# Kernel tuning notes

Measured on AMD Instinct MI355X. Metric: run time of the kernel, lower is better.

The kernel has to match this reference:

```python
import jax, jax.numpy as jnp
import numpy as np

D_MODEL = 768
N_HEADS = 4
N_POINTS = 4
PATCH = 16
IMG = 224
HF = IMG // PATCH  # 14
WF = IMG // PATCH  # 14
LQ = HF * WF       # 196 tokens
DH = D_MODEL // N_HEADS  # 192


def setup_inputs() -> dict:
    key = jax.random.key(0)
    ks = jax.random.split(key, 14)
    s = 0.02
    inp = {
        "x": jax.random.normal(ks[0], (4, 16, 3, IMG, IMG), dtype=jnp.float32),
        # patch-embed conv (Conv2d 3->768, k=16, s=16)
        "embed_w": s * jax.random.normal(ks[1], (D_MODEL, 3, PATCH, PATCH), dtype=jnp.float32),
        "embed_b": jnp.zeros((D_MODEL,), dtype=jnp.float32),
        # MSDeformAttn linears (nn.Linear stores W as [out, in]; y = x @ W.T + b)
        "value_w": s * jax.random.normal(ks[2], (D_MODEL, D_MODEL), dtype=jnp.float32),
        "value_b": jnp.zeros((D_MODEL,), dtype=jnp.float32),
        "off_w": s * jax.random.normal(ks[3], (N_HEADS * N_POINTS * 2, D_MODEL), dtype=jnp.float32),
        "off_b": s * jax.random.normal(ks[4], (N_HEADS * N_POINTS * 2,), dtype=jnp.float32),
        "aw_w": s * jax.random.normal(ks[5], (N_HEADS * N_POINTS, D_MODEL), dtype=jnp.float32),
        "aw_b": jnp.zeros((N_HEADS * N_POINTS,), dtype=jnp.float32),
        "outp_w": s * jax.random.normal(ks[6], (D_MODEL, D_MODEL), dtype=jnp.float32),
        "outp_b": jnp.zeros((D_MODEL,), dtype=jnp.float32),
        # final nn.Linear proj
        "proj_w": s * jax.random.normal(ks[7], (D_MODEL, D_MODEL), dtype=jnp.float32),
        "proj_b": jnp.zeros((D_MODEL,), dtype=jnp.float32),
    }
    return inp


def _patch_embed(x, w, b):
    # x: (N,3,H,W); non-overlapping 16x16 patches == Conv2d(3,D,16,16)
    N = x.shape[0]
    xh = x.reshape(N, 3, HF, PATCH, WF, PATCH)
    feat = jnp.einsum('nchpwq,dcpq->nhwd', xh, w) + b  # (N,HF,WF,D)
    return feat.reshape(N, LQ, D_MODEL)


def _ref_points():
    lin = jnp.linspace(0.0, 1.0, HF)
    gy, gx = jnp.meshgrid(lin, lin, indexing='ij')
    return jnp.stack([gx, gy], -1).reshape(LQ, 2)  # (Lq, 2) in [0,1], (x,y)


def _deform_attn_core(value, loc, attn):
    # value: (N, Lq, M, Dh); loc: (N, Lq, M, P, 2) normalized [0,1]; attn: (N, Lq, M, P)
    N = value.shape[0]
    # grid_sample align_corners=False: pixel = (2*loc-1 + 1)*S/2 - 0.5 = loc*S - 0.5
    px = loc[..., 0] * WF - 0.5
    py = loc[..., 1] * HF - 0.5
    x0 = jnp.floor(px).astype(jnp.int32)
    y0 = jnp.floor(py).astype(jnp.int32)
    x1, y1 = x0 + 1, y0 + 1
    wx1 = px - x0.astype(px.dtype)
    wy1 = py - y0.astype(py.dtype)
    wx0, wy0 = 1.0 - wx1, 1.0 - wy1

    valh = value.transpose(0, 2, 1, 3)  # (N, M, HW, Dh)

    def gather(ix, iy):
        valid = (ix >= 0) & (ix < WF) & (iy >= 0) & (iy < HF)  # zeros padding
        idx = jnp.clip(iy, 0, HF - 1) * WF + jnp.clip(ix, 0, WF - 1)
        idxm = idx.transpose(0, 2, 1, 3).reshape(N, N_HEADS, LQ * N_POINTS)
        g = jnp.take_along_axis(valh, idxm[..., None], axis=2)  # (N,M,Lq*P,Dh)
        g = g * valid.transpose(0, 2, 1, 3).reshape(N, N_HEADS, LQ * N_POINTS, 1)
        return g.reshape(N, N_HEADS, LQ, N_POINTS, DH)

    def w4(a, b):  # (N,Lq,M,P) -> (N,M,Lq,P,1)
        return (a * b).transpose(0, 2, 1, 3)[..., None]

    sampled = (w4(wx0, wy0) * gather(x0, y0) + w4(wx1, wy0) * gather(x1, y0)
               + w4(wx0, wy1) * gather(x0, y1) + w4(wx1, wy1) * gather(x1, y1))
    # weighted combine over points
    out = (sampled * attn.transpose(0, 2, 1, 3)[..., None]).sum(3)  # (N,M,Lq,Dh)
    return out.transpose(0, 2, 1, 3).reshape(N, LQ, D_MODEL)


def reference(x, embed_w, embed_b, value_w, value_b, off_w, off_b, aw_w, aw_b,
              outp_w, outp_b, proj_w, proj_b):
    B, T = x.shape[0], x.shape[1]
    N = B * T
    xi = x.reshape(N, 3, IMG, IMG)
    feat = _patch_embed(xi, embed_w, embed_b)  # (N, Lq, D)

    # MSDeformAttn (n_levels=1)
    value = (feat @ value_w.T + value_b).reshape(N, LQ, N_HEADS, DH)
    off = (feat @ off_w.T + off_b).reshape(N, LQ, N_HEADS, N_POINTS, 2)
    aw = (feat @ aw_w.T + aw_b).reshape(N, LQ, N_HEADS, N_POINTS)
    aw = jax.nn.softmax(aw, axis=-1)  # softmax over n_levels*n_points = 4

    ref = _ref_points()  # (Lq, 2)
    norm = jnp.array([WF, HF], dtype=feat.dtype)  # offset_normalizer = (W, H)
    loc = ref[None, :, None, None, :] + off / norm  # (N,Lq,M,P,2)

    out = _deform_attn_core(value, loc, aw)
    out = out @ outp_w.T + outp_b  # output_proj

    pooled = out.mean(axis=1)  # mean over tokens
    final = pooled @ proj_w.T + proj_b
    return final.reshape(B, T, D_MODEL)
```

## Files before the change

### kernel.cpp

```cpp
#include <hip/hip_runtime.h>
#include <hip/hip_bf16.h>


using bf16 = __bf16;
typedef bf16  bf16x8 __attribute__((ext_vector_type(8)));
typedef float f32x4  __attribute__((ext_vector_type(4)));

#define N_IMG   64
#define LQ      196
#define DM      768
#define NH      4
#define DH      192
#define M_ROWS  (N_IMG * LQ)
#define NCAT    896

#define OFF_A     ((size_t)0)
#define OFF_FEAT  (OFF_A    + 19267584)
#define OFF_WEMB  (OFF_FEAT + 19267584)
#define OFF_WCAT  (OFF_WEMB + 1179648)
#define OFF_BCAT  (OFF_WCAT + 1376256)
#define OFF_VBUF  (OFF_BCAT + 4096)
#define OFF_OA    (OFF_VBUF + 19267584)
#define OFF_CORE  (OFF_OA   + 3211264)
#define OFF_POOL  (OFF_CORE + 196608)

__device__ __forceinline__ void gload_lds16(const bf16* g, bf16* l) {
#if __has_builtin(__builtin_amdgcn_global_load_lds)
  __builtin_amdgcn_global_load_lds(
      (const __attribute__((address_space(1))) void*)g,
      (__attribute__((address_space(3))) void*)l, 16, 0, 0);
#else
  *(bf16x8*)l = *(const bf16x8*)g;
#endif
}

__global__ void stage_kernel(const float* __restrict__ x,
                             const float* __restrict__ embed_w,
                             const float* __restrict__ value_w,
                             const float* __restrict__ off_w,
                             const float* __restrict__ aw_w,
                             const float* __restrict__ value_b,
                             const float* __restrict__ off_b,
                             const float* __restrict__ aw_b,
                             bf16* __restrict__ A,
                             bf16* __restrict__ Wemb, bf16* __restrict__ Wcat,
                             float* __restrict__ bcat, float* __restrict__ core) {
  const int bid = blockIdx.x;
  if (bid < 9408) {
    const int t   = bid * 256 + threadIdx.x;
    const int row = t / 192;
    const int j   = t - row * 192;
    const int k   = j * 4;
    const int c   = k >> 8;
    const int r   = k & 255;
    const int p   = r >> 4;
    const int q   = r & 15;
    const int n   = row / 196;
    const int lq  = row - n * 196;
    const int h   = lq / 14;
    const int w   = lq - h * 14;
    const float4 v = *(const float4*)(x +
        ((((size_t)n * 3 + c) * 224) + h * 16 + p) * 224 + w * 16 + q);
    bf16* dst = A + (size_t)row * DM + k;
    dst[0] = (bf16)v.x; dst[1] = (bf16)v.y; dst[2] = (bf16)v.z; dst[3] = (bf16)v.w;
    return;
  }
  const int idx = (bid - 9408) * 256 + threadIdx.x;
  if (idx < DM * DM) Wemb[idx] = (bf16)embed_w[idx];
  {
    int rr = idx / DM, kk = idx - rr * DM;
    float v = 0.f;
    if (rr < 768)       v = value_w[idx];
    else if (rr < 800)  v = off_w[(rr - 768) * DM + kk];
    else if (rr < 816)  v = aw_w[(rr - 800) * DM + kk];
    Wcat[idx] = (bf16)v;
  }
  if (idx < NCAT) {
    float v = 0.f;
    if (idx < 768)      v = value_b[idx];
    else if (idx < 800) v = off_b[idx - 768];
    else if (idx < 816) v = aw_b[idx - 800];
    bcat[idx] = v;
  }
  if (idx < N_IMG * DM) core[idx] = 0.f;
}

template <typename OutT>
__global__ void gemm_bt(const bf16* __restrict__ A, const bf16* __restrict__ B,
                        const float* __restrict__ bias, OutT* __restrict__ C,
                        int M, int N, int K) {
  __shared__ bf16 As[128 * 64];
  __shared__ bf16 Bs[128 * 64];

  const int tid  = threadIdx.x;
  const int wave = tid >> 6;
  const int lane = tid & 63;
  const int nBase = blockIdx.x * 128;
  const int mBase = blockIdx.y * 128;
  const int wm = wave & 1;
  const int wn = wave >> 1;
  const int quad = lane >> 4;
  const int r16  = lane & 15;

  const f32x4 zero = {0.f, 0.f, 0.f, 0.f};
  f32x4 acc[4][4];
#pragma unroll
  for (int mi = 0; mi < 4; ++mi)
#pragma unroll
    for (int ni = 0; ni < 4; ++ni) acc[mi][ni] = zero;

  const int srow = wave * 32 + (lane >> 3);
  const int scol = (lane & 7) * 8;
  const bf16* Ag = A + (size_t)(mBase + srow) * K + scol;
  const bf16* Bg = B + (size_t)(nBase + srow) * K + scol;
  bf16* Al = As + srow * 64 + scol;
  bf16* Bl = Bs + srow * 64 + scol;

  for (int kt = 0; kt < K; kt += 64) {
#pragma unroll
    for (int i = 0; i < 4; ++i) {
      gload_lds16(Ag + (size_t)(i * 8) * K + kt, Al + i * 8 * 64);
      gload_lds16(Bg + (size_t)(i * 8) * K + kt, Bl + i * 8 * 64);
    }
    __syncthreads();
#pragma unroll
    for (int kk = 0; kk < 64; kk += 32) {
      bf16x8 af[4], bfr[4];
#pragma unroll
      for (int mi = 0; mi < 4; ++mi)
        af[mi] = *(const bf16x8*)&As[(wm * 64 + mi * 16 + r16) * 64 + kk + quad * 8];
#pragma unroll
      for (int ni = 0; ni < 4; ++ni)
        bfr[ni] = *(const bf16x8*)&Bs[(wn * 64 + ni * 16 + r16) * 64 + kk + quad * 8];
#pragma unroll
      for (int mi = 0; mi < 4; ++mi)
#pragma unroll
        for (int ni = 0; ni < 4; ++ni)
          acc[mi][ni] = __builtin_amdgcn_mfma_f32_16x16x32_bf16(
              af[mi], bfr[ni], acc[mi][ni], 0, 0, 0);
    }
    __syncthreads();
  }

#pragma unroll
  for (int ni = 0; ni < 4; ++ni) {
    const int col = nBase + wn * 64 + ni * 16 + r16;
    const float bv = bias[col];
#pragma unroll
    for (int mi = 0; mi < 4; ++mi) {
      const int row0 = mBase + wm * 64 + mi * 16 + quad * 4;
#pragma unroll
      for (int rr = 0; rr < 4; ++rr) {
        float v = acc[mi][ni][rr] + bv;
        C[(size_t)(row0 + rr) * N + col] = (OutT)v;
      }
    }
  }
}

__global__ void gemm2_mixed(const bf16* __restrict__ A, const bf16* __restrict__ B,
                            const float* __restrict__ bias,
                            bf16* __restrict__ Vb, float* __restrict__ OA,
                            int M, int N, int K) {
  __shared__ bf16 As[128 * 64];
  __shared__ bf16 Bs[128 * 64];

  const int tid  = threadIdx.x;
  const int wave = tid >> 6;
  const int lane = tid & 63;
  const int nBase = blockIdx.x * 128;
  const int mBase = blockIdx.y * 128;
  const int wm = wave & 1;
  const int wn = wave >> 1;
  const int quad = lane >> 4;
  const int r16  = lane & 15;

  const f32x4 zero = {0.f, 0.f, 0.f, 0.f};
  f32x4 acc[4][4];
#pragma unroll
  for (int mi = 0; mi < 4; ++mi)
#pragma unroll
    for (int ni = 0; ni < 4; ++ni) acc[mi][ni] = zero;

  const int srow = wave * 32 + (lane >> 3);
  const int scol = (lane & 7) * 8;
  const bf16* Ag = A + (size_t)(mBase + srow) * K + scol;
  const bf16* Bg = B + (size_t)(nBase + srow) * K + scol;
  bf16* Al = As + srow * 64 + scol;
  bf16* Bl = Bs + srow * 64 + scol;

  for (int kt = 0; kt < K; kt += 64) {
#pragma unroll
    for (int i = 0; i < 4; ++i) {
      gload_lds16(Ag + (size_t)(i * 8) * K + kt, Al + i * 8 * 64);
      gload_lds16(Bg + (size_t)(i * 8) * K + kt, Bl + i * 8 * 64);
    }
    __syncthreads();
#pragma unroll
    for (int kk = 0; kk < 64; kk += 32) {
      bf16x8 af[4], bfr[4];
#pragma unroll
      for (int mi = 0; mi < 4; ++mi)
        af[mi] = *(const bf16x8*)&As[(wm * 64 + mi * 16 + r16) * 64 + kk + quad * 8];
#pragma unroll
      for (int ni = 0; ni < 4; ++ni)
        bfr[ni] = *(const bf16x8*)&Bs[(wn * 64 + ni * 16 + r16) * 64 + kk + quad * 8];
#pragma unroll
      for (int mi = 0; mi < 4; ++mi)
#pragma unroll
        for (int ni = 0; ni < 4; ++ni)
          acc[mi][ni] = __builtin_amdgcn_mfma_f32_16x16x32_bf16(
              af[mi], bfr[ni], acc[mi][ni], 0, 0, 0);
    }
    __syncthreads();
  }

#pragma unroll
  for (int ni = 0; ni < 4; ++ni) {
    const int col = nBase + wn * 64 + ni * 16 + r16;
    const float bv = bias[col];
#pragma unroll
    for (int mi = 0; mi < 4; ++mi) {
      const int row0 = mBase + wm * 64 + mi * 16 + quad * 4;
#pragma unroll
      for (int rr = 0; rr < 4; ++rr) {
        float v = acc[mi][ni][rr] + bv;
        int row = row0 + rr;
        if (col < 768) {
          Vb[(size_t)row * 768 + col] = (bf16)v;
        } else if (col < 816) {
          OA[(size_t)row * 64 + (col - 768)] = v;
        }
      }
    }
  }
}

__global__ void deform_kernel(const bf16* __restrict__ Vb,
                              const float* __restrict__ OA,
                              float* __restrict__ core) {
  __shared__ float s_w[64][4];
  __shared__ int   s_t[64][4];

  const int n   = blockIdx.x;
  const int lq0 = blockIdx.y * 4;
  const int z   = blockIdx.z;
  const int tid = threadIdx.x;

  if (tid < 64) {
    const int i = tid >> 4;
    const int m = (tid >> 2) & 3;
    const int p = tid & 3;
    const int lq = lq0 + i;
    const float* row = OA + ((size_t)n * LQ + lq) * 64;

    const float l0 = row[32 + m * 4 + 0];
    const float l1 = row[32 + m * 4 + 1];
    const float l2 = row[32 + m * 4 + 2];
    const float l3 = row[32 + m * 4 + 3];
    const float mx = fmaxf(fmaxf(l0, l1), fmaxf(l2, l3));
    const float e0 = __expf(l0 - mx), e1 = __expf(l1 - mx);
    const float e2 = __expf(l2 - mx), e3 = __expf(l3 - mx);
    const float inv = 1.f / (e0 + e1 + e2 + e3);
    const float ep[4] = {e0, e1, e2, e3};
    const float ew = ep[p] * inv;

    const int h = lq / 14, w = lq - (lq / 14) * 14;
    const float px = (float)w * (14.f / 13.f) - 0.5f + row[(m * 4 + p) * 2 + 0];
    const float py = (float)h * (14.f / 13.f) - 0.5f + row[(m * 4 + p) * 2 + 1];
    const float fx = floorf(px), fy = floorf(py);
    const int x0 = (int)fx, y0 = (int)fy;
    const float wx1 = px - fx, wy1 = py - fy;
    const float wx0 = 1.f - wx1, wy0 = 1.f - wy1;

    const bool vx0 = (x0 >= 0) & (x0 < 14);
    const bool vx1 = (x0 >= -1) & (x0 < 13);
    const bool vy0 = (y0 >= 0) & (y0 < 14);
    const bool vy1 = (y0 >= -1) & (y0 < 13);
    const int cx0 = min(max(x0, 0), 13),      cx1 = min(max(x0 + 1, 0), 13);
    const int cy0 = min(max(y0, 0), 13) * 14, cy1 = min(max(y0 + 1, 0), 13) * 14;

    s_w[tid][0] = (vx0 & vy0) ? ew * wx0 * wy0 : 0.f;
    s_w[tid][1] = (vx1 & vy0) ? ew * wx1 * wy0 : 0.f;
    s_w[tid][2] = (vx0 & vy1) ? ew * wx0 * wy1 : 0.f;
    s_w[tid][3] = (vx1 & vy1) ? ew * wx1 * wy1 : 0.f;
    s_t[tid][0] = cy0 + cx0;
    s_t[tid][1] = cy0 + cx1;
    s_t[tid][2] = cy1 + cx0;
    s_t[tid][3] = cy1 + cx1;
  }
  __syncthreads();

  const int ch = z * 256 + tid;
  const int m  = ch / DH;
  const bf16* vb = Vb + (size_t)n * LQ * 768 + ch;
  float acc = 0.f;
#pragma unroll
  for (int i = 0; i < 4; ++i) {
#pragma unroll
    for (int p = 0; p < 4; ++p) {
      const int e = i * 16 + m * 4 + p;
      const float4 w4 = *(const float4*)s_w[e];
      const int4   t4 = *(const int4*)s_t[e];
      acc += w4.x * (float)vb[(size_t)t4.x * 768];
      acc += w4.y * (float)vb[(size_t)t4.y * 768];
      acc += w4.z * (float)vb[(size_t)t4.z * 768];
      acc += w4.w * (float)vb[(size_t)t4.w * 768];
    }
  }
  atomicAdd(&core[(size_t)n * DM + ch], acc * (1.f / 196.f));
}

__global__ void small_linear(const float* __restrict__ in,
                             const float* __restrict__ W,
                             const float* __restrict__ b,
                             float* __restrict__ out) {
  const int n = blockIdx.x;
  const int d = blockIdx.y * 256 + threadIdx.x;
  const float4* a4 = (const float4*)(in + (size_t)n * DM);
  const float4* w4 = (const float4*)(W + (size_t)d * DM);
  float acc = 0.f;
#pragma unroll 4
  for (int k = 0; k < DM / 4; ++k) {
    float4 a = a4[k], w = w4[k];
    acc += a.x * w.x + a.y * w.y + a.z * w.z + a.w * w.w;
  }
  out[(size_t)n * DM + d] = acc + b[d];
}

extern "C" void kernel_launch(void* const* d_in, const int* in_sizes, int n_in,
                              void* d_out, int out_size, void* d_ws, size_t ws_size,
                              hipStream_t stream) {
  const float* x       = (const float*)d_in[0];
  const float* embed_w = (const float*)d_in[1];
  const float* embed_b = (const float*)d_in[2];
  const float* value_w = (const float*)d_in[3];
  const float* value_b = (const float*)d_in[4];
  const float* off_w   = (const float*)d_in[5];
  const float* off_b   = (const float*)d_in[6];
  const float* aw_w    = (const float*)d_in[7];
  const float* aw_b    = (const float*)d_in[8];
  const float* outp_w  = (const float*)d_in[9];
  const float* outp_b  = (const float*)d_in[10];
  const float* proj_w  = (const float*)d_in[11];
  const float* proj_b  = (const float*)d_in[12];
  float* out = (float*)d_out;

  char* ws = (char*)d_ws;
  bf16*  A      = (bf16*)(ws + OFF_A);
  bf16*  feat   = (bf16*)(ws + OFF_FEAT);
  bf16*  Wemb   = (bf16*)(ws + OFF_WEMB);
  bf16*  Wcat   = (bf16*)(ws + OFF_WCAT);
  float* bcat   = (float*)(ws + OFF_BCAT);
  bf16*  Vbuf   = (bf16*)(ws + OFF_VBUF);
  float* OA     = (float*)(ws + OFF_OA);
  float* core   = (float*)(ws + OFF_CORE);
  float* pooled = (float*)(ws + OFF_POOL);

  stage_kernel<<<dim3(12096), dim3(256), 0, stream>>>(
      x, embed_w, value_w, off_w, aw_w, value_b, off_b, aw_b,
      A, Wemb, Wcat, bcat, core);

  gemm_bt<bf16><<<dim3(DM / 128, M_ROWS / 128), dim3(256), 0, stream>>>(
      A, Wemb, embed_b, feat, M_ROWS, DM, DM);

  gemm2_mixed<<<dim3(NCAT / 128, M_ROWS / 128), dim3(256), 0, stream>>>(
      feat, Wcat, bcat, Vbuf, OA, M_ROWS, NCAT, DM);

  deform_kernel<<<dim3(N_IMG, 49, 3), dim3(256), 0, stream>>>(Vbuf, OA, core);

  small_linear<<<dim3(N_IMG, 3), dim3(256), 0, stream>>>(core, outp_w, outp_b, pooled);
  small_linear<<<dim3(N_IMG, 3), dim3(256), 0, stream>>>(pooled, proj_w, proj_b, out);
}
```

Before: 236.2 us.

## Fold patch-embed weights into value/offset/attention projection weights

Precomputes Wfused = Wcat @ Wemb and bfused = Wcat @ embed_b + bcat, so the per-token patch-embed GEMM (12544x768x768) is replaced by a small weight-only GEMM (896x768x768). The mixed GEMM then reads the raw patch matrix A directly, skipping one full activation GEMM and the write and read of the intermediate feat buffer. It adds a transpose of embed_w and a reduction kernel section for the fused bias, and changes rounding because the fused weights are rounded to bf16 once instead of feat being rounded.

```diff
diff --git a/kernel.cpp b/kernel.cpp
--- a/kernel.cpp
+++ b/kernel.cpp
@@ -14,15 +14,16 @@
 #define M_ROWS  (N_IMG * LQ)
 #define NCAT    896
 
-#define OFF_A     ((size_t)0)
-#define OFF_FEAT  (OFF_A    + 19267584)
-#define OFF_WEMB  (OFF_FEAT + 19267584)
-#define OFF_WCAT  (OFF_WEMB + 1179648)
-#define OFF_BCAT  (OFF_WCAT + 1376256)
-#define OFF_VBUF  (OFF_BCAT + 4096)
-#define OFF_OA    (OFF_VBUF + 19267584)
-#define OFF_CORE  (OFF_OA   + 3211264)
-#define OFF_POOL  (OFF_CORE + 196608)
+#define OFF_A      ((size_t)0)
+#define OFF_WEMBT  (OFF_A     + 19267584)
+#define OFF_WCAT   (OFF_WEMBT + 1179648)
+#define OFF_WFUSE  (OFF_WCAT  + 1376256)
+#define OFF_BFUSE  (OFF_WFUSE + 1376256)
+#define OFF_ZB     (OFF_BFUSE + 4096)
+#define OFF_VBUF   (OFF_ZB    + 4096)
+#define OFF_OA     (OFF_VBUF  + 19267584)
+#define OFF_CORE   (OFF_OA    + 3211264)
+#define OFF_POOL   (OFF_CORE  + 196608)
 
 __device__ __forceinline__ void gload_lds16(const bf16* g, bf16* l) {
 #if __has_builtin(__builtin_amdgcn_global_load_lds)
@@ -36,6 +37,7 @@
 
 __global__ void stage_kernel(const float* __restrict__ x,
                              const float* __restrict__ embed_w,
+                             const float* __restrict__ embed_b,
                              const float* __restrict__ value_w,
                              const float* __restrict__ off_w,
                              const float* __restrict__ aw_w,
@@ -43,8 +45,9 @@
                              const float* __restrict__ off_b,
                              const float* __restrict__ aw_b,
                              bf16* __restrict__ A,
-                             bf16* __restrict__ Wemb, bf16* __restrict__ Wcat,
-                             float* __restrict__ bcat, float* __restrict__ core) {
+                             bf16* __restrict__ WembT, bf16* __restrict__ Wcat,
+                             float* __restrict__ bfused, float* __restrict__ zb,
+                             float* __restrict__ core) {
   const int bid = blockIdx.x;
   if (bid < 9408) {
     const int t   = bid * 256 + threadIdx.x;
@@ -65,24 +68,39 @@
     dst[0] = (bf16)v.x; dst[1] = (bf16)v.y; dst[2] = (bf16)v.z; dst[3] = (bf16)v.w;
     return;
   }
-  const int idx = (bid - 9408) * 256 + threadIdx.x;
-  if (idx < DM * DM) Wemb[idx] = (bf16)embed_w[idx];
-  {
-    int rr = idx / DM, kk = idx - rr * DM;
-    float v = 0.f;
-    if (rr < 768)       v = value_w[idx];
-    else if (rr < 800)  v = off_w[(rr - 768) * DM + kk];
-    else if (rr < 816)  v = aw_w[(rr - 800) * DM + kk];
-    Wcat[idx] = (bf16)v;
-  }
-  if (idx < NCAT) {
-    float v = 0.f;
-    if (idx < 768)      v = value_b[idx];
-    else if (idx < 800) v = off_b[idx - 768];
-    else if (idx < 816) v = aw_b[idx - 800];
-    bcat[idx] = v;
-  }
-  if (idx < N_IMG * DM) core[idx] = 0.f;
+  if (bid < 12096) {
+    const int idx = (bid - 9408) * 256 + threadIdx.x;
+    {
+      int rr = idx / DM, kk = idx - rr * DM;
+      float v = 0.f;
+      if (rr < 768)       v = value_w[idx];
+      else if (rr < 800)  v = off_w[(rr - 768) * DM + kk];
+      else if (rr < 816)  v = aw_w[(rr - 800) * DM + kk];
+      Wcat[idx] = (bf16)v;
+    }
+    if (idx < DM * DM) {
+      int kk = idx / DM, jj = idx - kk * DM;
+      WembT[idx] = (bf16)embed_w[(size_t)jj * DM + kk];
+    }
+    if (idx < DM) zb[idx] = 0.f;
+    if (idx < N_IMG * DM) core[idx] = 0.f;
+    return;
+  }
+  const int t  = threadIdx.x;
+  const int r  = (bid - 12096) * 32 + (t >> 3);
+  const int t8 = t & 7;
+  const float* src = nullptr;
+  float badd = 0.f;
+  if (r < 768)      { src = value_w + (size_t)r * DM;        badd = value_b[r]; }
+  else if (r < 800) { src = off_w  + (size_t)(r - 768) * DM; badd = off_b[r - 768]; }
+  else if (r < 816) { src = aw_w   + (size_t)(r - 800) * DM; badd = aw_b[r - 800]; }
+  float s = 0.f;
+  if (src) {
+    for (int j = t8; j < DM; j += 8) s += src[j] * embed_b[j];
+  }
+#pragma unroll
+  for (int o = 4; o >= 1; o >>= 1) s += __shfl_down(s, o, 8);
+  if (t8 == 0) bfused[r] = (src ? s + badd : 0.f);
 }
 
 template <typename OutT>
@@ -348,24 +366,25 @@
 
   char* ws = (char*)d_ws;
   bf16*  A      = (bf16*)(ws + OFF_A);
-  bf16*  feat   = (bf16*)(ws + OFF_FEAT);
-  bf16*  Wemb   = (bf16*)(ws + OFF_WEMB);
+  bf16*  WembT  = (bf16*)(ws + OFF_WEMBT);
   bf16*  Wcat   = (bf16*)(ws + OFF_WCAT);
-  float* bcat   = (float*)(ws + OFF_BCAT);
+  bf16*  Wfused = (bf16*)(ws + OFF_WFUSE);
+  float* bfused = (float*)(ws + OFF_BFUSE);
+  float* zb     = (float*)(ws + OFF_ZB);
   bf16*  Vbuf   = (bf16*)(ws + OFF_VBUF);
   float* OA     = (float*)(ws + OFF_OA);
   float* core   = (float*)(ws + OFF_CORE);
   float* pooled = (float*)(ws + OFF_POOL);
 
-  stage_kernel<<<dim3(12096), dim3(256), 0, stream>>>(
-      x, embed_w, value_w, off_w, aw_w, value_b, off_b, aw_b,
-      A, Wemb, Wcat, bcat, core);
-
-  gemm_bt<bf16><<<dim3(DM / 128, M_ROWS / 128), dim3(256), 0, stream>>>(
-      A, Wemb, embed_b, feat, M_ROWS, DM, DM);
+  stage_kernel<<<dim3(12124), dim3(256), 0, stream>>>(
+      x, embed_w, embed_b, value_w, off_w, aw_w, value_b, off_b, aw_b,
+      A, WembT, Wcat, bfused, zb, core);
+
+  gemm_bt<bf16><<<dim3(DM / 128, NCAT / 128), dim3(256), 0, stream>>>(
+      Wcat, WembT, zb, Wfused, NCAT, DM, DM);
 
   gemm2_mixed<<<dim3(NCAT / 128, M_ROWS / 128), dim3(256), 0, stream>>>(
-      feat, Wcat, bcat, Vbuf, OA, M_ROWS, NCAT, DM);
+      A, Wfused, bfused, Vbuf, OA, M_ROWS, NCAT, DM);
 
   deform_kernel<<<dim3(N_IMG, 49, 3), dim3(256), 0, stream>>>(Vbuf, OA, core);
 
```

Result: slower. 247.9 us (+5.0%).
